# Kernel optimization log

Hardware: AMD Instinct MI355X
Metric: run time of the kernel (lower is better)

Reference implementation:

```python
import jax, jax.numpy as jnp
import numpy as np

B, E, IN, OUT = 512, 8, 1024, 1024


def setup_inputs() -> dict:
    key = jax.random.key(0)
    k1, k2, k3, k4 = jax.random.split(key, 4)
    x = jax.random.normal(k1, (B, IN), dtype=jnp.float32)
    expert_weights = jax.random.uniform(k2, (B, E), dtype=jnp.float32)
    # kaiming_uniform per expert with a=sqrt(5): bound = sqrt(6/((1+a^2)*fan_in)) = 1/sqrt(fan_in)
    wb = 1.0 / np.sqrt(IN)
    weight = jax.random.uniform(k3, (E, OUT, IN), dtype=jnp.float32, minval=-wb, maxval=wb)
    bias = jax.random.uniform(k4, (E, OUT), dtype=jnp.float32, minval=-wb, maxval=wb)
    return {"x": x, "expert_weights": expert_weights, "weight": weight, "bias": bias}


def reference(x, expert_weights, weight, bias):
    # Same math as: blended_W = einsum('bk,koi->boi'); bmm(blended_W, x[...,None]) + blended_b
    # fused as a single contraction to avoid the [B, out, in] intermediate.
    y = jnp.einsum('bk,koi,bi->bo', expert_weights, weight, x)
    b = jnp.einsum('bk,ko->bo', expert_weights, bias)
    return y + b
```

## Files before the change

kernel.cpp:

```cpp
#include <hip/hip_runtime.h>
#include <hip/hip_bf16.h>


#define EDIM 8
#define INDIM 1024
#define OUTDIM 1024
#define BATCH 512
#define TM 256
#define TNR 64
#define BK 64
#define NITER (INDIM / BK)

typedef __attribute__((ext_vector_type(8))) short frag8;
typedef __attribute__((ext_vector_type(4))) float f32x4;

__device__ inline void async_ld16(void* lds, const void* g) {
  __builtin_amdgcn_global_load_lds(
      (const __attribute__((address_space(1))) void*)g,
      (__attribute__((address_space(3))) void*)lds, 16, 0, 0);
}

__device__ inline ushort f2bf(float f) {
  unsigned u = __builtin_bit_cast(unsigned, f);
  u += 0x7fffu + ((u >> 16) & 1u);
  return (ushort)(u >> 16);
}

__device__ inline ushort4 f4_to_bf4(float4 v) {
  ushort4 o;
  o.x = f2bf(v.x); o.y = f2bf(v.y); o.z = f2bf(v.z); o.w = f2bf(v.w);
  return o;
}

__global__ __launch_bounds__(256) void prep_x(const float* __restrict__ x,
                                              ushort* __restrict__ wsX) {
  int i = blockIdx.x * 256 + threadIdx.x;
  float4 v = ((const float4*)x)[i];
  ((ushort4*)wsX)[i] = f4_to_bf4(v);
}

__global__ __launch_bounds__(512) void gemm_fused(
    const ushort* __restrict__ Xb,
    const float* __restrict__ ew,
    const float* __restrict__ W,
    const float* __restrict__ bias,
    float* __restrict__ out) {
  __shared__ __align__(16) ushort As[2][TM * BK];
  __shared__ __align__(16) ushort Bs[2][TNR * BK];

  const int tid  = threadIdx.x;
  const int lane = tid & 63;
  const int wave = tid >> 6;
  const int o0 = blockIdx.x * 8;
  const int m0 = blockIdx.y * TM;

  const int l15  = lane & 15;
  const int quad = lane >> 4;

  const ushort* aG = Xb + (size_t)(m0 + (lane >> 3)) * INDIM + (lane & 7) * 8;

  int fi0 = tid, fi1 = tid + 512;
  int r0 = fi0 >> 4, s0 = fi0 & 15;
  int r1 = fi1 >> 4, s1 = fi1 & 15;
  const float* bG0 = W + (size_t)((r0 >> 3) * 1024 + o0 + (r0 & 7)) * INDIM + s0 * 4;
  const float* bG1 = W + (size_t)((r1 >> 3) * 1024 + o0 + (r1 & 7)) * INDIM + s1 * 4;
  ushort* bW0base = &Bs[0][0] + r0 * BK + s0 * 4;
  ushort* bW1base = &Bs[0][0] + r1 * BK + s1 * 4;

  f32x4 acc[2][4] = {};

#pragma unroll
  for (int cc = 0; cc < 4; ++cc) {
    const int c = wave * 4 + cc;
    async_ld16(&As[0][c * 512], aG + (size_t)c * 8 * INDIM);
  }
  {
    float4 v0 = *(const float4*)bG0;
    float4 v1 = *(const float4*)bG1;
    *(ushort4*)bW0base = f4_to_bf4(v0);
    *(ushort4*)bW1base = f4_to_bf4(v1);
  }
  __syncthreads();

  for (int it = 0; it < NITER; ++it) {
    const int cur = it & 1, nxt = cur ^ 1;
    const bool more = (it + 1 < NITER);
    float4 v0, v1;
    if (more) {
      const int k0n = (it + 1) * BK;
#pragma unroll
      for (int cc = 0; cc < 4; ++cc) {
        const int c = wave * 4 + cc;
        async_ld16(&As[nxt][c * 512], aG + (size_t)c * 8 * INDIM + k0n);
      }
      v0 = *(const float4*)(bG0 + k0n);
      v1 = *(const float4*)(bG1 + k0n);
    }

#pragma unroll
    for (int kk = 0; kk < BK; kk += 32) {
      frag8 a[2], b[4];
#pragma unroll
      for (int i = 0; i < 2; ++i)
        a[i] = *(const frag8*)&As[cur][(wave * 32 + i * 16 + l15) * BK + kk + quad * 8];
#pragma unroll
      for (int j = 0; j < 4; ++j)
        b[j] = *(const frag8*)&Bs[cur][(j * 16 + l15) * BK + kk + quad * 8];
#pragma unroll
      for (int i = 0; i < 2; ++i)
#pragma unroll
        for (int j = 0; j < 4; ++j)
          acc[i][j] = __builtin_amdgcn_mfma_f32_16x16x32_bf16(a[i], b[j], acc[i][j], 0, 0, 0);
    }

    if (more) {
      *(ushort4*)(bW0base + nxt * (TNR * BK)) = f4_to_bf4(v0);
      *(ushort4*)(bW1base + nxt * (TNR * BK)) = f4_to_bf4(v1);
    }
    __syncthreads();
  }

  const int h  = l15 >> 3;
  const int oc = o0 + (l15 & 7);
  float bgather[4];
#pragma unroll
  for (int j = 0; j < 4; ++j) bgather[j] = bias[(2 * j + h) * OUTDIM + oc];

#pragma unroll
  for (int i = 0; i < 2; ++i) {
#pragma unroll
    for (int r = 0; r < 4; ++r) {
      const int b = m0 + wave * 32 + i * 16 + quad * 4 + r;
      float p = 0.f;
#pragma unroll
      for (int j = 0; j < 4; ++j)
        p += ew[b * EDIM + 2 * j + h] * (acc[i][j][r] + bgather[j]);
      p += __shfl_xor(p, 8, 64);
      if (h == 0) out[(size_t)b * OUTDIM + oc] = p;
    }
  }
}

__global__ __launch_bounds__(256) void fallback_kernel(
    const float* __restrict__ x, const float* __restrict__ ew,
    const float* __restrict__ W, const float* __restrict__ bias,
    float* __restrict__ out) {
  int idx = blockIdx.x * 256 + threadIdx.x;
  int b = idx >> 10;
  int o = idx & 1023;
  float y = 0.f;
  for (int k = 0; k < EDIM; ++k) {
    const float* wr = W + ((size_t)k * OUTDIM + o) * INDIM;
    const float* xr = x + (size_t)b * INDIM;
    float dot = 0.f;
    for (int i = 0; i < INDIM; ++i) dot += wr[i] * xr[i];
    y += ew[k + b * EDIM] * (dot + bias[k * OUTDIM + o]);
  }
  out[idx] = y;
}

extern "C" void kernel_launch(void* const* d_in, const int* in_sizes, int n_in,
                              void* d_out, int out_size, void* d_ws, size_t ws_size,
                              hipStream_t stream) {
  const float* x    = (const float*)d_in[0];
  const float* ew   = (const float*)d_in[1];
  const float* W    = (const float*)d_in[2];
  const float* bias = (const float*)d_in[3];
  float* out = (float*)d_out;

  if (ws_size < (size_t)(BATCH * INDIM * 2)) {
    fallback_kernel<<<2048, 256, 0, stream>>>(x, ew, W, bias, out);
    return;
  }
  ushort* wsX = (ushort*)d_ws;

  prep_x<<<512, 256, 0, stream>>>(x, wsX);
  gemm_fused<<<dim3(OUTDIM / 8, BATCH / TM), 512, 0, stream>>>(
      wsX, ew, W, bias, out);
}
```

Baseline: 105.6 us.

## Halve the M tile to 128 rows and XOR-swizzle LDS tiles to avoid bank conflicts

The batch tile shrinks from 256 to 128 rows and the block from 512 to 256 threads, with launch bounds asking for two blocks per CU. This doubles the grid and raises occupancy. Both the X and W tiles in LDS now use an XOR swizzle on the 16-byte k-slot, keyed by row, to cut bank conflicts on the fragment reads. The trade-off is that W is converted and loaded twice as often across M tiles, and each thread now issues four W loads per k-step instead of two.

```diff
diff --git a/kernel.cpp b/kernel.cpp
--- a/kernel.cpp
+++ b/kernel.cpp
@@ -6,7 +6,7 @@
 #define INDIM 1024
 #define OUTDIM 1024
 #define BATCH 512
-#define TM 256
+#define TM 128
 #define TNR 64
 #define BK 64
 #define NITER (INDIM / BK)
@@ -35,18 +35,17 @@
 __global__ __launch_bounds__(256) void prep_x(const float* __restrict__ x,
                                               ushort* __restrict__ wsX) {
   int i = blockIdx.x * 256 + threadIdx.x;
-  float4 v = ((const float4*)x)[i];
-  ((ushort4*)wsX)[i] = f4_to_bf4(v);
+  ((ushort4*)wsX)[i] = f4_to_bf4(((const float4*)x)[i]);
 }
 
-__global__ __launch_bounds__(512) void gemm_fused(
+__global__ __launch_bounds__(256, 2) void gemm_fused(
     const ushort* __restrict__ Xb,
     const float* __restrict__ ew,
     const float* __restrict__ W,
     const float* __restrict__ bias,
     float* __restrict__ out) {
-  __shared__ __align__(16) ushort As[2][TM * BK];
-  __shared__ __align__(16) ushort Bs[2][TNR * BK];
+  __shared__ __align__(16) ushort As[2 * TM * BK];
+  __shared__ __align__(16) ushort Bs[2 * TNR * BK];
 
   const int tid  = threadIdx.x;
   const int lane = tid & 63;
@@ -57,55 +56,63 @@
   const int l15  = lane & 15;
   const int quad = lane >> 4;
 
-  const ushort* aG = Xb + (size_t)(m0 + (lane >> 3)) * INDIM + (lane & 7) * 8;
+  const int arow   = lane >> 3;
+  const int akslot = (lane & 7) ^ arow;
+  const ushort* aG = Xb + (size_t)(m0 + arow) * INDIM + akslot * 8;
 
-  int fi0 = tid, fi1 = tid + 512;
-  int r0 = fi0 >> 4, s0 = fi0 & 15;
-  int r1 = fi1 >> 4, s1 = fi1 & 15;
-  const float* bG0 = W + (size_t)((r0 >> 3) * 1024 + o0 + (r0 & 7)) * INDIM + s0 * 4;
-  const float* bG1 = W + (size_t)((r1 >> 3) * 1024 + o0 + (r1 & 7)) * INDIM + s1 * 4;
-  ushort* bW0base = &Bs[0][0] + r0 * BK + s0 * 4;
-  ushort* bW1base = &Bs[0][0] + r1 * BK + s1 * 4;
+  const float* bG[4];
+  int bWoff[4];
+#pragma unroll
+  for (int p = 0; p < 4; ++p) {
+    int fi = tid + 256 * p;
+    int rb = fi >> 4, gs = fi & 15;
+    bG[p] = W + (size_t)((rb >> 3) * 1024 + o0 + (rb & 7)) * INDIM + gs * 4;
+    bWoff[p] = rb * 64 + (((gs >> 1) ^ (rb & 7)) * 8) + (gs & 1) * 4;
+  }
 
   f32x4 acc[2][4] = {};
 
 #pragma unroll
   for (int cc = 0; cc < 4; ++cc) {
-    const int c = wave * 4 + cc;
-    async_ld16(&As[0][c * 512], aG + (size_t)c * 8 * INDIM);
+    int c = wave * 4 + cc;
+    async_ld16(&As[c * 512], aG + (size_t)c * 8 * INDIM);
   }
-  {
-    float4 v0 = *(const float4*)bG0;
-    float4 v1 = *(const float4*)bG1;
-    *(ushort4*)bW0base = f4_to_bf4(v0);
-    *(ushort4*)bW1base = f4_to_bf4(v1);
-  }
+#pragma unroll
+  for (int p = 0; p < 4; ++p)
+    *(ushort4*)&Bs[bWoff[p]] = f4_to_bf4(*(const float4*)bG[p]);
   __syncthreads();
 
   for (int it = 0; it < NITER; ++it) {
     const int cur = it & 1, nxt = cur ^ 1;
     const bool more = (it + 1 < NITER);
-    float4 v0, v1;
+    float4 bv[4];
     if (more) {
-      const int k0n = (it + 1) * BK;
+      const int kn = (it + 1) * BK;
 #pragma unroll
       for (int cc = 0; cc < 4; ++cc) {
-        const int c = wave * 4 + cc;
-        async_ld16(&As[nxt][c * 512], aG + (size_t)c * 8 * INDIM + k0n);
+        int c = wave * 4 + cc;
+        async_ld16(&As[nxt * (TM * BK) + c * 512],
+                   aG + (size_t)c * 8 * INDIM + kn);
       }
-      v0 = *(const float4*)(bG0 + k0n);
-      v1 = *(const float4*)(bG1 + k0n);
+#pragma unroll
+      for (int p = 0; p < 4; ++p) bv[p] = *(const float4*)(bG[p] + kn);
     }
 
 #pragma unroll
-    for (int kk = 0; kk < BK; kk += 32) {
+    for (int kk8 = 0; kk8 < 8; kk8 += 4) {
       frag8 a[2], b[4];
 #pragma unroll
-      for (int i = 0; i < 2; ++i)
-        a[i] = *(const frag8*)&As[cur][(wave * 32 + i * 16 + l15) * BK + kk + quad * 8];
+      for (int i = 0; i < 2; ++i) {
+        int ra = wave * 32 + i * 16 + l15;
+        a[i] = *(const frag8*)&As[cur * (TM * BK) + ra * 64 +
+                                  (((quad + kk8) ^ (ra & 7)) * 8)];
+      }
 #pragma unroll
-      for (int j = 0; j < 4; ++j)
-        b[j] = *(const frag8*)&Bs[cur][(j * 16 + l15) * BK + kk + quad * 8];
+      for (int j = 0; j < 4; ++j) {
+        int rb = j * 16 + l15;
+        b[j] = *(const frag8*)&Bs[cur * (TNR * BK) + rb * 64 +
+                                  (((quad + kk8) ^ (rb & 7)) * 8)];
+      }
 #pragma unroll
       for (int i = 0; i < 2; ++i)
 #pragma unroll
@@ -114,17 +121,18 @@
     }
 
     if (more) {
-      *(ushort4*)(bW0base + nxt * (TNR * BK)) = f4_to_bf4(v0);
-      *(ushort4*)(bW1base + nxt * (TNR * BK)) = f4_to_bf4(v1);
+#pragma unroll
+      for (int p = 0; p < 4; ++p)
+        *(ushort4*)&Bs[nxt * (TNR * BK) + bWoff[p]] = f4_to_bf4(bv[p]);
     }
     __syncthreads();
   }
 
   const int h  = l15 >> 3;
   const int oc = o0 + (l15 & 7);
-  float bgather[4];
+  float bg[4];
 #pragma unroll
-  for (int j = 0; j < 4; ++j) bgather[j] = bias[(2 * j + h) * OUTDIM + oc];
+  for (int j = 0; j < 4; ++j) bg[j] = bias[(2 * j + h) * OUTDIM + oc];
 
 #pragma unroll
   for (int i = 0; i < 2; ++i) {
@@ -134,7 +142,7 @@
       float p = 0.f;
 #pragma unroll
       for (int j = 0; j < 4; ++j)
-        p += ew[b * EDIM + 2 * j + h] * (acc[i][j][r] + bgather[j]);
+        p += ew[b * EDIM + 2 * j + h] * (acc[i][j][r] + bg[j]);
       p += __shfl_xor(p, 8, 64);
       if (h == 0) out[(size_t)b * OUTDIM + oc] = p;
     }
@@ -154,7 +162,7 @@
     const float* xr = x + (size_t)b * INDIM;
     float dot = 0.f;
     for (int i = 0; i < INDIM; ++i) dot += wr[i] * xr[i];
-    y += ew[k + b * EDIM] * (dot + bias[k * OUTDIM + o]);
+    y += ew[b * EDIM + k] * (dot + bias[k * OUTDIM + o]);
   }
   out[idx] = y;
 }
@@ -175,6 +183,6 @@
   ushort* wsX = (ushort*)d_ws;
 
   prep_x<<<512, 256, 0, stream>>>(x, wsX);
-  gemm_fused<<<dim3(OUTDIM / 8, BATCH / TM), 512, 0, stream>>>(
+  gemm_fused<<<dim3(OUTDIM / 8, BATCH / TM), 256, 0, stream>>>(
       wsX, ew, W, bias, out);
 }
```

New measurement: 99.84 us, median of 2. 5.5% less time.
